# Performance work log

Hardware: AMD Instinct MI355X
Metric: run time of the kernel (lower is better)

The kernel has to match this reference:

```python
import jax, jax.numpy as jnp
import numpy as np

B, N_STATES, STATE_SIZE = 32768, 16, 32
ENC, HID, OUT = 64, 128, 8


def setup_inputs() -> dict:
    key = jax.random.key(0)
    ks = jax.random.split(key, 8)
    states = jax.random.normal(ks[0], (B, N_STATES, STATE_SIZE), dtype=jnp.float32)
    # validity flags: first element of each per-field state. agent state (index 0)
    # always valid; neighbor states valid with prob 0.7 (contiguity enforced in reference
    # via cumprod, matching the original while-loop semantics).
    flags = (jax.random.uniform(ks[1], (B, N_STATES)) < 0.7).astype(jnp.float32)
    flags = flags.at[:, 0].set(1.0)
    states = states.at[:, :, 0].set(flags)
    obs_flat = states.reshape(B, N_STATES * STATE_SIZE)
    s = 0.05
    return {
        "obs_flat": obs_flat,
        "W_enc": jax.random.normal(ks[2], (STATE_SIZE, ENC), dtype=jnp.float32) * s,
        "b_enc": jnp.zeros((ENC,), dtype=jnp.float32),
        "W_f": jax.random.normal(ks[3], (2 * ENC, HID), dtype=jnp.float32) * s,
        "b_f": jnp.zeros((HID,), dtype=jnp.float32),
        "W_dec": jax.random.normal(ks[4], (HID, OUT), dtype=jnp.float32) * s,
        "b_dec": jnp.zeros((OUT,), dtype=jnp.float32),
    }


def reference(obs_flat, W_enc, b_enc, W_f, b_f, W_dec, b_dec):
    Bsz = obs_flat.shape[0]
    states = obs_flat.reshape(Bsz, N_STATES, STATE_SIZE)          # [B,N,S]
    flags = states[:, :, 0]                                        # [B,N]
    # original: while-loop stops at first invalid state -> contiguous-prefix validity
    neigh_valid = jnp.cumprod((flags[:, 1:] == 1.0).astype(jnp.float32), axis=1)  # [B,N-1]
    enc = jax.nn.relu(jnp.einsum('bns,se->bne', states, W_enc) + b_enc)            # [B,N,E]
    agent_enc = enc[:, 0]                                          # [B,E]
    neigh_enc = enc[:, 1:]                                         # [B,N-1,E]
    cnt = jnp.sum(neigh_valid, axis=1)                             # [B]
    # mean aggregation over valid neighbors; zero vector if none (original aggregates [zeros])
    agg = jnp.einsum('bne,bn->be', neigh_enc, neigh_valid) / jnp.maximum(cnt, 1.0)[:, None]
    f_in = jnp.concatenate([agent_enc, agg], axis=-1)              # [B,2E]
    hidden = jax.nn.relu(f_in @ W_f + b_f)                         # [B,H]
    logits = hidden @ W_dec + b_dec                                # [B,O]
    return logits
```

## Files before the change

kernel.cpp:

```cpp
#include <hip/hip_runtime.h>
#include <stdint.h>

#define NB    32768
#define NS    16
#define SS    32
#define ENCD  64
#define HIDD  128
#define OUTD  8
#define BT    16
#define THREADS 256

typedef _Float16 half8 __attribute__((ext_vector_type(8)));
typedef float    f32x4 __attribute__((ext_vector_type(4)));

#define MFMA(a, b, c) __builtin_amdgcn_mfma_f32_16x16x32_f16((a), (b), (c), 0, 0, 0)

__device__ __forceinline__ half8 pack8(const float* f) {
  half8 h;
#pragma unroll
  for (int j = 0; j < 8; ++j) h[j] = (_Float16)f[j];
  return h;
}

__global__ __launch_bounds__(THREADS, 6)
void gnn_fused(const float* __restrict__ obs,
               const float* __restrict__ W_enc,
               const float* __restrict__ b_enc,
               const float* __restrict__ W_f,
               const float* __restrict__ b_f,
               const float* __restrict__ W_dec,
               const float* __restrict__ b_dec,
               float* __restrict__ out)
{
  __shared__ __align__(16) _Float16 f_in[BT][136];
  __shared__ __align__(16) _Float16 hidn[BT][136];

  const int tid  = threadIdx.x;
  const int w    = tid >> 6;
  const int l    = tid & 63;
  const int m15  = l & 15;
  const int quad = l >> 4;
  const int b0   = blockIdx.x * BT;

  half8 we[4];
  float benc[4];
#pragma unroll
  for (int nt = 0; nt < 4; ++nt) {
    float f[8];
#pragma unroll
    for (int j = 0; j < 8; ++j)
      f[j] = W_enc[(size_t)(quad * 8 + j) * ENCD + nt * 16 + m15];
    we[nt]   = pack8(f);
    benc[nt] = b_enc[nt * 16 + m15];
  }

  const float* bp = obs + (size_t)(b0 + w * 4) * (NS * SS) + m15 * SS + quad * 8;
  float4 c0[4], c1[4];
#pragma unroll
  for (int i = 0; i < 4; ++i) {
    const float* p = bp + (size_t)i * (NS * SS);
    c0[i] = ((const float4*)p)[0];
    c1[i] = ((const float4*)p)[1];
  }
#pragma unroll
  for (int i = 0; i < 4; ++i) {
    float f[8] = {c0[i].x, c0[i].y, c0[i].z, c0[i].w,
                  c1[i].x, c1[i].y, c1[i].z, c1[i].w};

    unsigned long long bal = __ballot((l < 16) && (f[0] == 1.0f));
    int run = __builtin_ctzll(~(bal >> 1));
    float inv = 1.0f / fmaxf((float)run, 1.0f);

    half8 a = pack8(f);

    const int bi = w * 4 + i;
#pragma unroll
    for (int nt = 0; nt < 4; ++nt) {
      f32x4 acc = {0.f, 0.f, 0.f, 0.f};
      acc = MFMA(a, we[nt], acc);
      float s = 0.f, e0 = 0.f;
#pragma unroll
      for (int r = 0; r < 4; ++r) {
        int n = quad * 4 + r;
        float v = fmaxf(acc[r] + benc[nt], 0.f);
        if (n == 0) e0 = v;
        if (n >= 1 && n <= run) s += v;
      }
      s += __shfl_xor(s, 16, 64);
      s += __shfl_xor(s, 32, 64);
      if (quad == 0) {
        f_in[bi][nt * 16 + m15]      = (_Float16)e0;
        f_in[bi][64 + nt * 16 + m15] = (_Float16)(s * inv);
      }
    }
  }
  __syncthreads();

  {
    half8 fa[4];
#pragma unroll
    for (int ks = 0; ks < 4; ++ks)
      fa[ks] = *(const half8*)&f_in[m15][ks * 32 + quad * 8];

#pragma unroll
    for (int tt = 0; tt < 2; ++tt) {
      const int h0 = (w * 2 + tt) * 16 + m15;
      f32x4 acc = {0.f, 0.f, 0.f, 0.f};
#pragma unroll
      for (int ks = 0; ks < 4; ++ks) {
        float f[8];
#pragma unroll
        for (int j = 0; j < 8; ++j)
          f[j] = W_f[(size_t)(ks * 32 + quad * 8 + j) * HIDD + h0];
        acc = MFMA(fa[ks], pack8(f), acc);
      }
      const float bfv = b_f[h0];
#pragma unroll
      for (int r = 0; r < 4; ++r)
        hidn[quad * 4 + r][h0] = (_Float16)fmaxf(acc[r] + bfv, 0.f);
    }
  }
  __syncthreads();

  if (w == 0) {
    half8 ga[4];
#pragma unroll
    for (int ks = 0; ks < 4; ++ks)
      ga[ks] = *(const half8*)&hidn[m15][ks * 32 + quad * 8];
    f32x4 acc = {0.f, 0.f, 0.f, 0.f};
#pragma unroll
    for (int ks = 0; ks < 4; ++ks) {
      float f[8];
#pragma unroll
      for (int j = 0; j < 8; ++j) {
        int k = ks * 32 + quad * 8 + j;
        f[j] = (m15 < OUTD) ? W_dec[(size_t)k * OUTD + m15] : 0.f;
      }
      acc = MFMA(ga[ks], pack8(f), acc);
    }
    if (m15 < OUTD) {
      const float bd = b_dec[m15];
#pragma unroll
      for (int r = 0; r < 4; ++r) {
        const int m = quad * 4 + r;
        out[(size_t)(b0 + m) * OUTD + m15] = acc[r] + bd;
      }
    }
  }
}

extern "C" void kernel_launch(void* const* d_in, const int* in_sizes, int n_in,
                              void* d_out, int out_size, void* d_ws, size_t ws_size,
                              hipStream_t stream) {
  (void)in_sizes; (void)n_in; (void)d_ws; (void)ws_size; (void)out_size;
  const float* obs   = (const float*)d_in[0];
  const float* W_enc = (const float*)d_in[1];
  const float* b_enc = (const float*)d_in[2];
  const float* W_f   = (const float*)d_in[3];
  const float* b_f   = (const float*)d_in[4];
  const float* W_dec = (const float*)d_in[5];
  const float* b_dec = (const float*)d_in[6];
  float* out = (float*)d_out;

  gnn_fused<<<dim3(NB / BT), dim3(THREADS), 0, stream>>>(
      obs, W_enc, b_enc, W_f, b_f, W_dec, b_dec, out);
}
```

Baseline: 114.1 us.

## Use single-wave blocks with prefetched rolling obs loads and preloaded decoder weights

Each block now runs one 64-lane wavefront that handles all 16 batch rows itself, instead of four waves handling four rows each. Obs rows are loaded through a 4-deep rolling register prefetch. The wave computes all 8 hidden tiles, and W_dec is packed into registers up front so its load is issued early. This cuts idle waves in the later stages and the block-level barrier cost. In exchange each wave does more serial work and there is less parallelism per block, relying on many resident blocks to hide memory latency.

```diff
diff --git a/kernel.cpp b/kernel.cpp
--- a/kernel.cpp
+++ b/kernel.cpp
@@ -8,7 +8,7 @@
 #define HIDD  128
 #define OUTD  8
 #define BT    16
-#define THREADS 256
+#define THREADS 64
 
 typedef _Float16 half8 __attribute__((ext_vector_type(8)));
 typedef float    f32x4 __attribute__((ext_vector_type(4)));
@@ -22,7 +22,7 @@
   return h;
 }
 
-__global__ __launch_bounds__(THREADS, 6)
+__global__ __launch_bounds__(THREADS, 2)
 void gnn_fused(const float* __restrict__ obs,
                const float* __restrict__ W_enc,
                const float* __restrict__ b_enc,
@@ -35,14 +35,21 @@
   __shared__ __align__(16) _Float16 f_in[BT][136];
   __shared__ __align__(16) _Float16 hidn[BT][136];
 
-  const int tid  = threadIdx.x;
-  const int w    = tid >> 6;
-  const int l    = tid & 63;
+  const int l    = threadIdx.x;
   const int m15  = l & 15;
   const int quad = l >> 4;
   const int b0   = blockIdx.x * BT;
 
-  half8 we[4];
+  const float* bp = obs + (size_t)b0 * (NS * SS) + m15 * SS + quad * 8;
+  float4 s0[4], s1[4];
+#pragma unroll
+  for (int d = 0; d < 4; ++d) {
+    const float* p = bp + (size_t)d * (NS * SS);
+    s0[d] = ((const float4*)p)[0];
+    s1[d] = ((const float4*)p)[1];
+  }
+
+  half8 we[4], wd[4];
   float benc[4];
 #pragma unroll
   for (int nt = 0; nt < 4; ++nt) {
@@ -53,27 +60,31 @@
     we[nt]   = pack8(f);
     benc[nt] = b_enc[nt * 16 + m15];
   }
+#pragma unroll
+  for (int ks = 0; ks < 4; ++ks) {
+    float f[8];
+#pragma unroll
+    for (int j = 0; j < 8; ++j)
+      f[j] = (m15 < OUTD) ? W_dec[(size_t)(ks * 32 + quad * 8 + j) * OUTD + m15] : 0.f;
+    wd[ks] = pack8(f);
+  }
 
-  const float* bp = obs + (size_t)(b0 + w * 4) * (NS * SS) + m15 * SS + quad * 8;
-  float4 c0[4], c1[4];
-#pragma unroll
-  for (int i = 0; i < 4; ++i) {
-    const float* p = bp + (size_t)i * (NS * SS);
-    c0[i] = ((const float4*)p)[0];
-    c1[i] = ((const float4*)p)[1];
-  }
-#pragma unroll
-  for (int i = 0; i < 4; ++i) {
-    float f[8] = {c0[i].x, c0[i].y, c0[i].z, c0[i].w,
-                  c1[i].x, c1[i].y, c1[i].z, c1[i].w};
+#pragma unroll 4
+  for (int i = 0; i < BT; ++i) {
+    const int sl = i & 3;
+    float f[8] = {s0[sl].x, s0[sl].y, s0[sl].z, s0[sl].w,
+                  s1[sl].x, s1[sl].y, s1[sl].z, s1[sl].w};
+    if (i + 4 < BT) {
+      const float* p = bp + (size_t)(i + 4) * (NS * SS);
+      s0[sl] = ((const float4*)p)[0];
+      s1[sl] = ((const float4*)p)[1];
+    }
 
     unsigned long long bal = __ballot((l < 16) && (f[0] == 1.0f));
     int run = __builtin_ctzll(~(bal >> 1));
     float inv = 1.0f / fmaxf((float)run, 1.0f);
 
     half8 a = pack8(f);
-
-    const int bi = w * 4 + i;
 #pragma unroll
     for (int nt = 0; nt < 4; ++nt) {
       f32x4 acc = {0.f, 0.f, 0.f, 0.f};
@@ -89,8 +100,8 @@
       s += __shfl_xor(s, 16, 64);
       s += __shfl_xor(s, 32, 64);
       if (quad == 0) {
-        f_in[bi][nt * 16 + m15]      = (_Float16)e0;
-        f_in[bi][64 + nt * 16 + m15] = (_Float16)(s * inv);
+        f_in[i][nt * 16 + m15]      = (_Float16)e0;
+        f_in[i][64 + nt * 16 + m15] = (_Float16)(s * inv);
       }
     }
   }
@@ -103,8 +114,8 @@
       fa[ks] = *(const half8*)&f_in[m15][ks * 32 + quad * 8];
 
 #pragma unroll
-    for (int tt = 0; tt < 2; ++tt) {
-      const int h0 = (w * 2 + tt) * 16 + m15;
+    for (int tt = 0; tt < 8; ++tt) {
+      const int h0 = tt * 16 + m15;
       f32x4 acc = {0.f, 0.f, 0.f, 0.f};
 #pragma unroll
       for (int ks = 0; ks < 4; ++ks) {
@@ -122,22 +133,15 @@
   }
   __syncthreads();
 
-  if (w == 0) {
+  {
     half8 ga[4];
 #pragma unroll
     for (int ks = 0; ks < 4; ++ks)
       ga[ks] = *(const half8*)&hidn[m15][ks * 32 + quad * 8];
     f32x4 acc = {0.f, 0.f, 0.f, 0.f};
 #pragma unroll
-    for (int ks = 0; ks < 4; ++ks) {
-      float f[8];
-#pragma unroll
-      for (int j = 0; j < 8; ++j) {
-        int k = ks * 32 + quad * 8 + j;
-        f[j] = (m15 < OUTD) ? W_dec[(size_t)k * OUTD + m15] : 0.f;
-      }
-      acc = MFMA(ga[ks], pack8(f), acc);
-    }
+    for (int ks = 0; ks < 4; ++ks)
+      acc = MFMA(ga[ks], wd[ks], acc);
     if (m15 < OUTD) {
       const float bd = b_dec[m15];
 #pragma unroll
```

After: 122.9 us. 1.08x slower.

## Double batch tile to 32 rows with 8 waves and reuse W_f fragments

Applied to the files above, without the earlier changes.

Raises the per-block batch tile from 16 to 32 rows and the block from 256 to 512 threads, so each wave loads its W_f column slice once and reuses it across two row tiles instead of reloading per output tile. Observation loads are issued first and converted to fp16 right away, which lowers register pressure, and the validity flag test now runs on the fp16 value. The decoder stage now runs on two waves. This halves the number of blocks and the per-block weight reloads, at the cost of larger blocks and a launch bound asking for 8 blocks per CU.

```diff
diff --git a/kernel.cpp b/kernel.cpp
--- a/kernel.cpp
+++ b/kernel.cpp
@@ -7,8 +7,8 @@
 #define ENCD  64
 #define HIDD  128
 #define OUTD  8
-#define BT    16
-#define THREADS 256
+#define BT    32
+#define THREADS 512
 
 typedef _Float16 half8 __attribute__((ext_vector_type(8)));
 typedef float    f32x4 __attribute__((ext_vector_type(4)));
@@ -22,7 +22,7 @@
   return h;
 }
 
-__global__ __launch_bounds__(THREADS, 6)
+__global__ __launch_bounds__(THREADS, 8)
 void gnn_fused(const float* __restrict__ obs,
                const float* __restrict__ W_enc,
                const float* __restrict__ b_enc,
@@ -42,6 +42,17 @@
   const int quad = l >> 4;
   const int b0   = blockIdx.x * BT;
 
+  const float* bp = obs + (size_t)(b0 + w * 4) * (NS * SS) + m15 * SS + quad * 8;
+  half8 a4[4];
+#pragma unroll
+  for (int d = 0; d < 4; ++d) {
+    const float* p = bp + (size_t)d * (NS * SS);
+    float4 c0 = ((const float4*)p)[0];
+    float4 c1 = ((const float4*)p)[1];
+    float f[8] = {c0.x, c0.y, c0.z, c0.w, c1.x, c1.y, c1.z, c1.w};
+    a4[d] = pack8(f);
+  }
+
   half8 we[4];
   float benc[4];
 #pragma unroll
@@ -54,30 +65,17 @@
     benc[nt] = b_enc[nt * 16 + m15];
   }
 
-  const float* bp = obs + (size_t)(b0 + w * 4) * (NS * SS) + m15 * SS + quad * 8;
-  float4 c0[4], c1[4];
 #pragma unroll
   for (int i = 0; i < 4; ++i) {
-    const float* p = bp + (size_t)i * (NS * SS);
-    c0[i] = ((const float4*)p)[0];
-    c1[i] = ((const float4*)p)[1];
-  }
-#pragma unroll
-  for (int i = 0; i < 4; ++i) {
-    float f[8] = {c0[i].x, c0[i].y, c0[i].z, c0[i].w,
-                  c1[i].x, c1[i].y, c1[i].z, c1[i].w};
-
-    unsigned long long bal = __ballot((l < 16) && (f[0] == 1.0f));
+    unsigned long long bal = __ballot((l < 16) && (a4[i][0] == (_Float16)1.0f));
     int run = __builtin_ctzll(~(bal >> 1));
     float inv = 1.0f / fmaxf((float)run, 1.0f);
-
-    half8 a = pack8(f);
 
     const int bi = w * 4 + i;
 #pragma unroll
     for (int nt = 0; nt < 4; ++nt) {
       f32x4 acc = {0.f, 0.f, 0.f, 0.f};
-      acc = MFMA(a, we[nt], acc);
+      acc = MFMA(a4[i], we[nt], acc);
       float s = 0.f, e0 = 0.f;
 #pragma unroll
       for (int r = 0; r < 4; ++r) {
@@ -97,36 +95,34 @@
   __syncthreads();
 
   {
-    half8 fa[4];
+    const int h0 = w * 16 + m15;
+    half8 wf[4];
 #pragma unroll
-    for (int ks = 0; ks < 4; ++ks)
-      fa[ks] = *(const half8*)&f_in[m15][ks * 32 + quad * 8];
+    for (int ks = 0; ks < 4; ++ks) {
+      float f[8];
+#pragma unroll
+      for (int j = 0; j < 8; ++j)
+        f[j] = W_f[(size_t)(ks * 32 + quad * 8 + j) * HIDD + h0];
+      wf[ks] = pack8(f);
+    }
+    const float bfv = b_f[h0];
 
 #pragma unroll
-    for (int tt = 0; tt < 2; ++tt) {
-      const int h0 = (w * 2 + tt) * 16 + m15;
+    for (int mt = 0; mt < 2; ++mt) {
       f32x4 acc = {0.f, 0.f, 0.f, 0.f};
 #pragma unroll
       for (int ks = 0; ks < 4; ++ks) {
-        float f[8];
-#pragma unroll
-        for (int j = 0; j < 8; ++j)
-          f[j] = W_f[(size_t)(ks * 32 + quad * 8 + j) * HIDD + h0];
-        acc = MFMA(fa[ks], pack8(f), acc);
+        half8 fa = *(const half8*)&f_in[mt * 16 + m15][ks * 32 + quad * 8];
+        acc = MFMA(fa, wf[ks], acc);
       }
-      const float bfv = b_f[h0];
 #pragma unroll
       for (int r = 0; r < 4; ++r)
-        hidn[quad * 4 + r][h0] = (_Float16)fmaxf(acc[r] + bfv, 0.f);
+        hidn[mt * 16 + quad * 4 + r][h0] = (_Float16)fmaxf(acc[r] + bfv, 0.f);
     }
   }
   __syncthreads();
 
-  if (w == 0) {
-    half8 ga[4];
-#pragma unroll
-    for (int ks = 0; ks < 4; ++ks)
-      ga[ks] = *(const half8*)&hidn[m15][ks * 32 + quad * 8];
+  if (w < 2) {
     f32x4 acc = {0.f, 0.f, 0.f, 0.f};
 #pragma unroll
     for (int ks = 0; ks < 4; ++ks) {
@@ -136,13 +132,14 @@
         int k = ks * 32 + quad * 8 + j;
         f[j] = (m15 < OUTD) ? W_dec[(size_t)k * OUTD + m15] : 0.f;
       }
-      acc = MFMA(ga[ks], pack8(f), acc);
+      half8 ga = *(const half8*)&hidn[w * 16 + m15][ks * 32 + quad * 8];
+      acc = MFMA(ga, pack8(f), acc);
     }
     if (m15 < OUTD) {
       const float bd = b_dec[m15];
 #pragma unroll
       for (int r = 0; r < 4; ++r) {
-        const int m = quad * 4 + r;
+        const int m = w * 16 + quad * 4 + r;
         out[(size_t)(b0 + m) * OUTD + m15] = acc[r] + bd;
       }
     }
```

Measured after the change: 131.9 us. +15.6%, slower.
